# Optimization experiments

Hardware: AMD Instinct MI355X
Metric: run time of the kernel (lower is better)

## Reference

```python
import jax, jax.numpy as jnp
import numpy as np

D = 2048; H = 16; DH = D // H; FF = 8192; PFF = 1024
EPS = 1e-6; THETA = 10000.0; CAPACITY = 0.5
BETA_CE = 1.0; BETA_CU = 1.0
SCALE = 0.02

def rms(x, w):
    return x * jax.lax.rsqrt(jnp.mean(x * x, axis=-1, keepdims=True) + EPS) * w

def rope(x, pos):
    # x: [B,H,T,DH], pos: [T]
    inv = 1.0 / (THETA ** (jnp.arange(0, DH, 2, dtype=jnp.float32) / DH))
    ang = pos[:, None] * inv[None, :]                      # [T, DH/2]
    cos = jnp.concatenate([jnp.cos(ang)] * 2, -1)          # [T, DH]
    sin = jnp.concatenate([jnp.sin(ang)] * 2, -1)
    x1, x2 = jnp.split(x, 2, axis=-1)
    rot = jnp.concatenate([-x2, x1], -1)
    return x * cos + rot * sin

def attention(x, wq, wk, wv, wo):
    B, T, _ = x.shape
    pos = jnp.arange(T, dtype=jnp.float32)
    q = (x @ wq).reshape(B, T, H, DH).transpose(0, 2, 1, 3)
    k = (x @ wk).reshape(B, T, H, DH).transpose(0, 2, 1, 3)
    v = (x @ wv).reshape(B, T, H, DH).transpose(0, 2, 1, 3)
    q = rope(q, pos); k = rope(k, pos)
    scores = jnp.einsum('bhqd,bhkd->bhqk', q, k) / np.sqrt(DH).astype(np.float32)
    mask = jnp.tril(jnp.ones((T, T), dtype=bool))
    scores = jnp.where(mask, scores, jnp.finfo(scores.dtype).min)
    probs = jax.nn.softmax(scores, axis=-1)
    out = jnp.einsum('bhqk,bhkd->bhqd', probs, v)
    return out.transpose(0, 2, 1, 3).reshape(B, T, D) @ wo

def swiglu(x, wg, wu, wd):
    return (jax.nn.silu(x @ wg) * (x @ wu)) @ wd

def decoder_layer(x, ln1, ln2, wq, wk, wv, wo, wg, wu, wd):
    h = x + attention(rms(x, ln1), wq, wk, wv, wo)
    return h + swiglu(rms(h, ln2), wg, wu, wd)

def setup_inputs() -> dict:
    key = jax.random.key(0)
    ks = iter(jax.random.split(key, 32))
    def w(shape):
        return SCALE * jax.random.normal(next(ks), shape, dtype=jnp.float32)
    inp = {'hidden_states': jax.random.normal(next(ks), (2, 2048, D), dtype=jnp.float32)}
    for p in ('d1', 'd2'):
        inp[p + '_ln1'] = jnp.ones((D,), jnp.float32)
        inp[p + '_ln2'] = jnp.ones((D,), jnp.float32)
        inp[p + '_wq'] = w((D, D)); inp[p + '_wk'] = w((D, D))
        inp[p + '_wv'] = w((D, D)); inp[p + '_wo'] = w((D, D))
        inp[p + '_wg'] = w((D, FF)); inp[p + '_wu'] = w((D, FF)); inp[p + '_wd'] = w((FF, D))
    inp['p_ln'] = jnp.ones((D,), jnp.float32)
    inp['p_wg'] = w((D, PFF)); inp['p_wu'] = w((D, PFF)); inp['p_wd'] = w((PFF, D))
    return inp

def reference(hidden_states,
              d1_ln1, d1_ln2, d1_wq, d1_wk, d1_wv, d1_wo, d1_wg, d1_wu, d1_wd,
              d2_ln1, d2_ln2, d2_wq, d2_wk, d2_wv, d2_wo, d2_wg, d2_wu, d2_wd,
              p_ln, p_wg, p_wu, p_wd):
    x = hidden_states
    B, T, _ = x.shape
    # decision layer: full decoder block + prior network
    processed = decoder_layer(x, d1_ln1, d1_ln2, d1_wq, d1_wk, d1_wv, d1_wo, d1_wg, d1_wu, d1_wd)
    prior_out = swiglu(rms(x, p_ln), p_wg, p_wu, p_wd)
    prior_hidden = x + prior_out
    actual_res = processed - x                 # [B,T,D]
    pred_res = prior_out                       # prior_hidden - x
    prior_loss = jnp.mean((prior_hidden - jax.lax.stop_gradient(processed)) ** 2)
    # surprise router (VPR-style gate)
    D_st = jnp.mean(actual_res ** 2, axis=-1)                    # [B,T]
    D_ch = jnp.mean((actual_res - pred_res) ** 2, axis=-1)       # [B,T]
    g_cont = jax.nn.sigmoid(BETA_CU * D_ch - BETA_CE * D_st)     # [B,T]
    # top-k token selection per batch row
    k = max(1, int(T * CAPACITY))
    gating_scores, topk_idx = jax.lax.top_k(g_cont, k)           # [B,k]
    # gather -> process through dynamic block -> soft-gate -> scatter
    sel = jnp.take_along_axis(processed, topk_idx[..., None], axis=1)   # [B,k,D]
    sel_out = decoder_layer(sel, d2_ln1, d2_ln2, d2_wq, d2_wk, d2_wv, d2_wo, d2_wg, d2_wu, d2_wd)
    updated = sel + gating_scores[..., None] * (sel_out - sel)   # soft gating (training)
    batch_idx = jnp.arange(B)[:, None]
    final = processed.at[batch_idx, topk_idx].set(updated)
    return final, prior_loss, g_cont
```

## Files before the change

### kernel.cpp

```cpp
#include <hip/hip_runtime.h>
#include <math.h>

#define D_    2048
#define H_    16
#define DH_   128
#define FF_   8192
#define PFF_  1024
#define B_    2
#define T_    2048
#define NTOK_ 4096
#define T2_   1024
#define NSEL_ 2048
#define EPS_  1e-6f
#define SCALE_QK 0.08838834764831845f

typedef __attribute__((ext_vector_type(8))) short bf16x8;
typedef __attribute__((ext_vector_type(4))) float f32x4;
typedef __attribute__((ext_vector_type(8))) unsigned short ushort8;

__device__ __forceinline__ float silu_f(float x) {
    return x / (1.0f + expf(-x));
}

__device__ __forceinline__ unsigned short bf16_rne(float f) {
    unsigned int u = __float_as_uint(f);
    unsigned int r = (u + 0x7fffu + ((u >> 16) & 1u)) >> 16;
    return (unsigned short)r;
}
__device__ __forceinline__ float bf16_tof(unsigned short h) {
    return __uint_as_float(((unsigned int)h) << 16);
}

__global__ __launch_bounds__(256) void rms_kernel(const float* __restrict__ x,
                                                  const float* __restrict__ w,
                                                  float* __restrict__ out) {
    int row = blockIdx.x;
    int tid = threadIdx.x;
    const float4* xr = (const float4*)(x + (size_t)row * D_);
    float4* orow = (float4*)(out + (size_t)row * D_);
    const float4* w4 = (const float4*)w;
    float4 v0 = xr[tid], v1 = xr[tid + 256];
    float s = v0.x*v0.x + v0.y*v0.y + v0.z*v0.z + v0.w*v0.w
            + v1.x*v1.x + v1.y*v1.y + v1.z*v1.z + v1.w*v1.w;
    __shared__ float red[256];
    red[tid] = s; __syncthreads();
    for (int off = 128; off > 0; off >>= 1) {
        if (tid < off) red[tid] += red[tid + off];
        __syncthreads();
    }
    float r = 1.0f / sqrtf(red[0] * (1.0f/2048.0f) + EPS_);
    float4 w0 = w4[tid], w1 = w4[tid + 256];
    float4 o0, o1;
    o0.x = v0.x*r*w0.x; o0.y = v0.y*r*w0.y; o0.z = v0.z*r*w0.z; o0.w = v0.w*r*w0.w;
    o1.x = v1.x*r*w1.x; o1.y = v1.y*r*w1.y; o1.z = v1.z*r*w1.z; o1.w = v1.w*r*w1.w;
    orow[tid] = o0; orow[tid + 256] = o1;
}

__global__ __launch_bounds__(256) void splitw_kernel(const float* __restrict__ W,
                                                     unsigned short* __restrict__ phi,
                                                     unsigned short* __restrict__ plo,
                                                     int K, int N) {
    __shared__ float Ts[64][68];
    int n0 = blockIdx.x << 6, k0 = blockIdx.y << 6;
    int tid = threadIdx.x;
#pragma unroll
    for (int it = 0; it < 4; ++it) {
        int idx = tid + (it << 8);
        int kr = idx >> 4, c4 = idx & 15;
        float4 v = *(const float4*)(W + (size_t)(k0 + kr) * N + n0 + (c4 << 2));
        Ts[kr][c4*4+0] = v.x; Ts[kr][c4*4+1] = v.y; Ts[kr][c4*4+2] = v.z; Ts[kr][c4*4+3] = v.w;
    }
    __syncthreads();
#pragma unroll
    for (int h = 0; h < 2; ++h) {
        int c = tid + (h << 8);
        int kc = c >> 6, n = c & 63;
        ushort8 hi, lo;
#pragma unroll
        for (int q = 0; q < 8; ++q) {
            float v = Ts[kc*8 + q][n];
            unsigned short hb = bf16_rne(v);
            hi[q] = hb;
            lo[q] = bf16_rne(v - bf16_tof(hb));
        }
        size_t off = ((size_t)((k0 >> 3) + kc) * N + (n0 + n)) * 8;
        *(ushort8*)(phi + off) = hi;
        *(ushort8*)(plo + off) = lo;
    }
}

__global__ __launch_bounds__(256) void splita_kernel(const float* __restrict__ A,
                                                     unsigned short* __restrict__ phi,
                                                     unsigned short* __restrict__ plo,
                                                     int M, int K) {
    __shared__ float Ts[64][68];
    int m0 = blockIdx.x << 6, k0 = blockIdx.y << 6;
    int tid = threadIdx.x;
#pragma unroll
    for (int it = 0; it < 4; ++it) {
        int idx = tid + (it << 8);
        int mr = idx >> 4, c4 = idx & 15;
        float4 v = *(const float4*)(A + (size_t)(m0 + mr) * K + k0 + (c4 << 2));
        Ts[mr][c4*4+0] = v.x; Ts[mr][c4*4+1] = v.y; Ts[mr][c4*4+2] = v.z; Ts[mr][c4*4+3] = v.w;
    }
    __syncthreads();
#pragma unroll
    for (int h = 0; h < 2; ++h) {
        int c = tid + (h << 8);
        int kc = c >> 6, m = c & 63;
        const float* src = &Ts[m][kc << 3];
        ushort8 hi, lo;
#pragma unroll
        for (int q = 0; q < 8; ++q) {
            float v = src[q];
            unsigned short hb = bf16_rne(v);
            hi[q] = hb;
            lo[q] = bf16_rne(v - bf16_tof(hb));
        }
        size_t off = ((size_t)((k0 >> 3) + kc) * M + (m0 + m)) * 8;
        *(ushort8*)(phi + off) = hi;
        *(ushort8*)(plo + off) = lo;
    }
}

__device__ __forceinline__ void stage_panel(unsigned short* lds,
                                            const unsigned short* __restrict__ panel,
                                            int ktile, int R, int brow, int tid) {
#pragma unroll
    for (int h = 0; h < 2; ++h) {
        int c = tid + (h << 8);
        const unsigned short* g = panel + ((size_t)((ktile << 2) + (c >> 7)) * R + (brow + (c & 127))) * 8;
        __builtin_amdgcn_global_load_lds((const __attribute__((address_space(1))) void*)g,
                                         (__attribute__((address_space(3))) void*)(lds + (size_t)c * 8),
                                         16, 0, 0);
    }
}

template<int NP, int EPI>
__global__ __launch_bounds__(256) void gemm_mfma(const unsigned short* __restrict__ pah,
                                                 const unsigned short* __restrict__ pal,
                                                 const unsigned short* __restrict__ pbh,
                                                 const unsigned short* __restrict__ pbl,
                                                 float* __restrict__ C,
                                                 const float* __restrict__ Rg,
                                                 unsigned short* __restrict__ Cph,
                                                 unsigned short* __restrict__ Cpl,
                                                 int M, int N, int K) {
    constexpr int NPAN = (NP == 3) ? 2 : 1;
    __shared__ __align__(16) unsigned short As[2][NPAN][4][128][8];
    __shared__ __align__(16) unsigned short Bs[2][NPAN][4][128][8];
    const int tid = threadIdx.x;
    int nwg = gridDim.x * gridDim.y;
    int wg = blockIdx.y * gridDim.x + blockIdx.x;
    if ((nwg & 7) == 0) {
        int cpx = nwg >> 3;
        wg = (wg & 7) * cpx + (wg >> 3);
    }
    const int bxs = wg % gridDim.x, bys = wg / gridDim.x;
    const int bm = bys << 7, bn = bxs << 7;
    const int lane = tid & 63, wave = tid >> 6;
    const int wm = (wave >> 1) << 6, wn = (wave & 1) << 6;
    const int fr = lane & 15, fk = lane >> 4;

    f32x4 acc[4][4];
#pragma unroll
    for (int i = 0; i < 4; ++i)
#pragma unroll
        for (int j = 0; j < 4; ++j) acc[i][j] = (f32x4)0.0f;

    const int nkt = K >> 5;

    stage_panel(&As[0][0][0][0][0], pah, 0, M, bm, tid);
    if (NP == 3) stage_panel(&As[0][1][0][0][0], pal, 0, M, bm, tid);
    stage_panel(&Bs[0][0][0][0][0], pbh, 0, N, bn, tid);
    if (NP == 3) stage_panel(&Bs[0][1][0][0][0], pbl, 0, N, bn, tid);
    __syncthreads();

    int cur = 0;
    for (int kt = 0; kt < nkt; ++kt) {
        if (kt + 1 < nkt) {
            int nxt = cur ^ 1;
            stage_panel(&As[nxt][0][0][0][0], pah, kt + 1, M, bm, tid);
            if (NP == 3) stage_panel(&As[nxt][1][0][0][0], pal, kt + 1, M, bm, tid);
            stage_panel(&Bs[nxt][0][0][0][0], pbh, kt + 1, N, bn, tid);
            if (NP == 3) stage_panel(&Bs[nxt][1][0][0][0], pbl, kt + 1, N, bn, tid);
        }

        bf16x8 ah[4], bh[4], al[4], bl[4];
#pragma unroll
        for (int i = 0; i < 4; ++i) {
            ah[i] = *(const bf16x8*)&As[cur][0][fk][wm + (i << 4) + fr][0];
            if (NP == 3) al[i] = *(const bf16x8*)&As[cur][NPAN-1][fk][wm + (i << 4) + fr][0];
        }
#pragma unroll
        for (int j = 0; j < 4; ++j) {
            bh[j] = *(const bf16x8*)&Bs[cur][0][fk][wn + (j << 4) + fr][0];
            if (NP == 3) bl[j] = *(const bf16x8*)&Bs[cur][NPAN-1][fk][wn + (j << 4) + fr][0];
        }
#pragma unroll
        for (int i = 0; i < 4; ++i)
#pragma unroll
            for (int j = 0; j < 4; ++j) {
                acc[i][j] = __builtin_amdgcn_mfma_f32_16x16x32_bf16(ah[i], bh[j], acc[i][j], 0, 0, 0);
                if (NP == 3) {
                    acc[i][j] = __builtin_amdgcn_mfma_f32_16x16x32_bf16(ah[i], bl[j], acc[i][j], 0, 0, 0);
                    acc[i][j] = __builtin_amdgcn_mfma_f32_16x16x32_bf16(al[i], bh[j], acc[i][j], 0, 0, 0);
                }
            }
        __syncthreads();
        cur ^= 1;
    }

#pragma unroll
    for (int i = 0; i < 4; ++i) {
        int row0 = bm + wm + (i << 4) + (fk << 2);
#pragma unroll
        for (int j = 0; j < 4; ++j) {
            int col = bn + wn + (j << 4) + fr;
#pragma unroll
            for (int r = 0; r < 4; ++r) {
                int row = row0 + r;
                size_t off = (size_t)row * N + col;
                float v = acc[i][j][r];
                if (EPI == 0) {
                    C[off] = v;
                } else if (EPI == 1) {
                    C[off] = v + Rg[off];
                } else if (EPI == 2) {
                    C[off] = silu_f(Rg[off]) * v;
                } else {
                    v = silu_f(Rg[off]) * v;
                    unsigned short hb = bf16_rne(v);
                    size_t poff = (((size_t)(col >> 3)) * M + row) * 8 + (col & 7);
                    Cph[poff] = hb;
                    if (EPI == 3) Cpl[poff] = bf16_rne(v - bf16_tof(hb));
                }
            }
        }
    }
}

__global__ __launch_bounds__(256) void rope_split_kernel(const float* __restrict__ X,
                                                         unsigned short* __restrict__ xh,
                                                         unsigned short* __restrict__ xl,
                                                         int seqmask, float scale) {
    int tok = blockIdx.x;
    int tid = threadIdx.x;
    int h = tid >> 4, d0 = (tid & 15) << 3;
    int pos = tok & seqmask;
    const float* src = X + (size_t)tok * D_ + h * DH_;
    bool lohalf = d0 < 64;
    float out[8];
#pragma unroll
    for (int q = 0; q < 8; ++q) {
        int d = d0 + q;
        int i = lohalf ? d : (d - 64);
        float e = (float)(2 * i) * (1.0f / 128.0f);
        float inv = 1.0f / powf(10000.0f, e);
        float ang = (float)pos * inv;
        float c = cosf(ang), s = sinf(ang);
        float x1 = src[i], x2 = src[i + 64];
        out[q] = lohalf ? (x1 * c - x2 * s) : (x2 * c + x1 * s);
    }
    ushort8 hi, lo;
#pragma unroll
    for (int q = 0; q < 8; ++q) {
        float v = out[q] * scale;
        unsigned short hb = bf16_rne(v);
        hi[q] = hb;
        lo[q] = bf16_rne(v - bf16_tof(hb));
    }
    size_t off = (size_t)tok * D_ + h * DH_ + d0;
    *(ushort8*)(xh + off) = hi;
    *(ushort8*)(xl + off) = lo;
}

__global__ __launch_bounds__(256) void vpack_kernel(const float* __restrict__ V,
                                                    unsigned short* __restrict__ vth,
                                                    unsigned short* __restrict__ vtl,
                                                    int T) {
    __shared__ float Ts[64][132];
    int kt = blockIdx.x, bh = blockIdx.y;
    int b = bh >> 4, h = bh & 15;
    int tid = threadIdx.x;
#pragma unroll
    for (int it = 0; it < 8; ++it) {
        int idx = tid + (it << 8);
        int r = idx >> 5, c4 = idx & 31;
        float4 v = *(const float4*)(V + ((size_t)(b * T + kt * 64 + r)) * D_ + h * DH_ + (c4 << 2));
        Ts[r][c4*4+0] = v.x; Ts[r][c4*4+1] = v.y; Ts[r][c4*4+2] = v.z; Ts[r][c4*4+3] = v.w;
    }
    __syncthreads();
    size_t obase = ((size_t)bh * (size_t)(T >> 3) + (size_t)kt * 8) * 1024;
#pragma unroll
    for (int it = 0; it < 4; ++it) {
        int c = tid + (it << 8);
        int kc = c >> 7, dh = c & 127;
        ushort8 hi, lo;
#pragma unroll
        for (int q = 0; q < 8; ++q) {
            float v = Ts[kc * 8 + q][dh];
            unsigned short hb = bf16_rne(v);
            hi[q] = hb;
            lo[q] = bf16_rne(v - bf16_tof(hb));
        }
        *(ushort8*)(vth + obase + (size_t)kc * 1024 + dh * 8) = hi;
        *(ushort8*)(vtl + obase + (size_t)kc * 1024 + dh * 8) = lo;
    }
}

__global__ __launch_bounds__(256) void attn_mfma(const unsigned short* __restrict__ QH,
                                                 const unsigned short* __restrict__ QL,
                                                 const unsigned short* __restrict__ KH,
                                                 const unsigned short* __restrict__ KL,
                                                 const unsigned short* __restrict__ VTH,
                                                 const unsigned short* __restrict__ VTL,
                                                 float* __restrict__ O, int T) {
    __shared__ __align__(16) unsigned short KV[16384];
    __shared__ __align__(16) float Ss[4096];
    __shared__ __align__(16) float mrow[64];
    __shared__ __align__(16) float lrow[64];
    __shared__ __align__(16) float crow[64];

    const int tid = threadIdx.x;
    const int qt = blockIdx.x, bh = blockIdx.y;
    const int b = bh >> 4, h = bh & 15;
    const int lane = tid & 63, w = tid >> 6;
    const int fr = lane & 15, fk = lane >> 4;
    const size_t tok0 = (size_t)b * T;

    char* lds_kv = (char*)&KV[0];
    char* lds_sp = (char*)&Ss[0];

    bf16x8 qfh[4], qfl[4];
    {
        const size_t qoff = (tok0 + (size_t)qt * 64 + w * 16 + fr) * D_ + h * DH_ + fk * 8;
#pragma unroll
        for (int ks = 0; ks < 4; ++ks) {
            qfh[ks] = *(const bf16x8*)(QH + qoff + ks * 32);
            qfl[ks] = *(const bf16x8*)(QL + qoff + ks * 32);
        }
    }
    if (tid < 64) { mrow[tid] = -1e30f; lrow[tid] = 0.f; }

    f32x4 acc[8];
#pragma unroll
    for (int nt = 0; nt < 8; ++nt) acc[nt] = (f32x4)0.f;

    const int srow = tid >> 2, sslot = tid & 3;
    const size_t vbase = (size_t)bh * (size_t)(T >> 3) * 1024;

    for (int kt = 0; kt <= qt; ++kt) {
        __syncthreads();
#pragma unroll
        for (int it = 0; it < 4; ++it) {
            int c = tid + (it << 8);
            int t = c >> 4;
            int sp = (c & 15) ^ (t & 7);
            size_t goff = (tok0 + (size_t)kt * 64 + t) * D_ + h * DH_ + sp * 8;
            __builtin_amdgcn_global_load_lds((const __attribute__((address_space(1))) void*)(KH + goff),
                (__attribute__((address_space(3))) void*)(lds_kv + c * 16), 16, 0, 0);
            __builtin_amdgcn_global_load_lds((const __attribute__((address_space(1))) void*)(KL + goff),
                (__attribute__((address_space(3))) void*)(lds_kv + 16384 + c * 16), 16, 0, 0);
        }
        __syncthreads();
        {
            f32x4 s[4];
#pragma unroll
            for (int nt = 0; nt < 4; ++nt) s[nt] = (f32x4)0.f;
#pragma unroll
            for (int ks = 0; ks < 4; ++ks) {
#pragma unroll
                for (int nt = 0; nt < 4; ++nt) {
                    int n = nt * 16 + fr;
                    int offk = (n * 256 + ks * 64 + fk * 16) ^ ((n & 7) << 4);
                    bf16x8 kfh = *(const bf16x8*)(lds_kv + offk);
                    bf16x8 kfl = *(const bf16x8*)(lds_kv + 16384 + offk);
                    s[nt] = __builtin_amdgcn_mfma_f32_16x16x32_bf16(qfh[ks], kfh, s[nt], 0, 0, 0);
                    s[nt] = __builtin_amdgcn_mfma_f32_16x16x32_bf16(qfh[ks], kfl, s[nt], 0, 0, 0);
                    s[nt] = __builtin_amdgcn_mfma_f32_16x16x32_bf16(qfl[ks], kfh, s[nt], 0, 0, 0);
                }
            }
#pragma unroll
            for (int nt = 0; nt < 4; ++nt)
#pragma unroll
                for (int r = 0; r < 4; ++r) {
                    int row = w * 16 + fk * 4 + r;
                    int col = nt * 16 + fr;
                    *(float*)(lds_sp + ((row * 256 + col * 4) ^ ((row & 7) << 4))) = s[nt][r];
                }
        }
        __syncthreads();
#pragma unroll
        for (int it = 0; it < 4; ++it) {
            int c = tid + (it << 8);
            size_t goff = vbase + (size_t)kt * 8192 + (size_t)c * 8;
            __builtin_amdgcn_global_load_lds((const __attribute__((address_space(1))) void*)(VTH + goff),
                (__attribute__((address_space(3))) void*)(lds_kv + c * 16), 16, 0, 0);
            __builtin_amdgcn_global_load_lds((const __attribute__((address_space(1))) void*)(VTL + goff),
                (__attribute__((address_space(3))) void*)(lds_kv + 16384 + c * 16), 16, 0, 0);
        }
        float p[16];
        float newm, psum, cr, oldl;
        {
            float tmax = -1e30f;
            int colbase = sslot * 16;
#pragma unroll
            for (int q4 = 0; q4 < 4; ++q4) {
                f32x4 sv = *(const f32x4*)(lds_sp + ((srow * 256 + sslot * 64 + q4 * 16) ^ ((srow & 7) << 4)));
#pragma unroll
                for (int e = 0; e < 4; ++e) {
                    float v = sv[e];
                    if (kt == qt && (colbase + q4 * 4 + e) > srow) v = -1e30f;
                    p[q4 * 4 + e] = v;
                    tmax = fmaxf(tmax, v);
                }
            }
            tmax = fmaxf(tmax, __shfl_xor(tmax, 1, 64));
            tmax = fmaxf(tmax, __shfl_xor(tmax, 2, 64));
            float oldm = mrow[srow];
            oldl = lrow[srow];
            newm = fmaxf(oldm, tmax);
            psum = 0.f;
#pragma unroll
            for (int e = 0; e < 16; ++e) { p[e] = expf(p[e] - newm); psum += p[e]; }
            psum += __shfl_xor(psum, 1, 64);
            psum += __shfl_xor(psum, 2, 64);
            cr = expf(oldm - newm);
        }
        __syncthreads();
        {
            ushort8 h0, h1, l0, l1;
#pragma unroll
            for (int e = 0; e < 8; ++e) {
                unsigned short hb = bf16_rne(p[e]);
                h0[e] = hb; l0[e] = bf16_rne(p[e] - bf16_tof(hb));
                unsigned short hb2 = bf16_rne(p[8 + e]);
                h1[e] = hb2; l1[e] = bf16_rne(p[8 + e] - bf16_tof(hb2));
            }
            int base = srow * 128 + sslot * 32;
            int swz = (srow & 7) << 4;
            *(ushort8*)(lds_sp + (base ^ swz)) = h0;
            *(ushort8*)(lds_sp + ((base + 16) ^ swz)) = h1;
            *(ushort8*)(lds_sp + 8192 + (base ^ swz)) = l0;
            *(ushort8*)(lds_sp + 8192 + ((base + 16) ^ swz)) = l1;
            if (sslot == 0) { mrow[srow] = newm; lrow[srow] = oldl * cr + psum; crow[srow] = cr; }
        }
        __syncthreads();
        {
            f32x4 crv = *(const f32x4*)&crow[w * 16 + fk * 4];
#pragma unroll
            for (int nt = 0; nt < 8; ++nt)
#pragma unroll
                for (int r = 0; r < 4; ++r) acc[nt][r] *= crv[r];
            int m = w * 16 + fr;
#pragma unroll
            for (int ks = 0; ks < 2; ++ks) {
                int offp = (m * 128 + ks * 64 + fk * 16) ^ ((m & 7) << 4);
                bf16x8 pfh = *(const bf16x8*)(lds_sp + offp);
                bf16x8 pfl = *(const bf16x8*)(lds_sp + 8192 + offp);
#pragma unroll
                for (int nt = 0; nt < 8; ++nt) {
                    int offv = (ks * 4 + fk) * 2048 + (nt * 16 + fr) * 16;
                    bf16x8 vfh = *(const bf16x8*)(lds_kv + offv);
                    bf16x8 vfl = *(const bf16x8*)(lds_kv + 16384 + offv);
                    acc[nt] = __builtin_amdgcn_mfma_f32_16x16x32_bf16(pfh, vfh, acc[nt], 0, 0, 0);
                    acc[nt] = __builtin_amdgcn_mfma_f32_16x16x32_bf16(pfh, vfl, acc[nt], 0, 0, 0);
                    acc[nt] = __builtin_amdgcn_mfma_f32_16x16x32_bf16(pfl, vfh, acc[nt], 0, 0, 0);
                }
            }
        }
    }
    __syncthreads();
    {
        f32x4 lv = *(const f32x4*)&lrow[w * 16 + fk * 4];
        float* orow = O + (tok0 + (size_t)qt * 64 + w * 16 + fk * 4) * D_ + h * DH_;
#pragma unroll
        for (int r = 0; r < 4; ++r) {
            float inv = 1.0f / lv[r];
#pragma unroll
            for (int nt = 0; nt < 8; ++nt)
                orow[(size_t)r * D_ + nt * 16 + fr] = acc[nt][r] * inv;
        }
    }
}

template<int EPI>
__global__ __launch_bounds__(256) void gemm128(const float* __restrict__ A,
                                               const float* __restrict__ Bm,
                                               float* __restrict__ C,
                                               const float* __restrict__ Rg,
                                               int M, int N, int K) {
    __shared__ float Ast[16][132];
    __shared__ float Bs[16][132];
    int bm = blockIdx.y << 7, bn = blockIdx.x << 7;
    int tid = threadIdx.x;
    int ty = tid >> 4, tx = tid & 15;
    float acc[8][8];
#pragma unroll
    for (int i = 0; i < 8; ++i)
#pragma unroll
        for (int j = 0; j < 8; ++j) acc[i][j] = 0.f;

    for (int k0 = 0; k0 < K; k0 += 16) {
#pragma unroll
        for (int it = 0; it < 2; ++it) {
            int idx = tid + (it << 8);
            int ar = idx >> 2, ac = idx & 3;
            float4 av = *(const float4*)(A + (size_t)(bm + ar) * K + k0 + (ac << 2));
            Ast[ac*4+0][ar] = av.x; Ast[ac*4+1][ar] = av.y;
            Ast[ac*4+2][ar] = av.z; Ast[ac*4+3][ar] = av.w;
            int br = idx >> 5, bc = idx & 31;
            float4 bv = *(const float4*)(Bm + (size_t)(k0 + br) * N + bn + (bc << 2));
            *(float4*)&Bs[br][bc << 2] = bv;
        }
        __syncthreads();
#pragma unroll
        for (int kk = 0; kk < 16; ++kk) {
            float a[8], b[8];
            *(float4*)&a[0] = *(const float4*)&Ast[kk][ty*4];
            *(float4*)&a[4] = *(const float4*)&Ast[kk][64 + ty*4];
            *(float4*)&b[0] = *(const float4*)&Bs[kk][tx*4];
            *(float4*)&b[4] = *(const float4*)&Bs[kk][64 + tx*4];
#pragma unroll
            for (int i = 0; i < 8; ++i)
#pragma unroll
                for (int j = 0; j < 8; ++j)
                    acc[i][j] += a[i] * b[j];
        }
        __syncthreads();
    }
#pragma unroll
    for (int i = 0; i < 8; ++i) {
        int row = bm + ((i < 4) ? (ty*4 + i) : (64 + ty*4 + (i - 4)));
#pragma unroll
        for (int half = 0; half < 2; ++half) {
            int col = bn + half*64 + tx*4;
            size_t off = (size_t)row * N + col;
            const float* ap = &acc[i][half*4];
            float4 r;
            if (EPI == 0) {
                r.x = ap[0]; r.y = ap[1]; r.z = ap[2]; r.w = ap[3];
            } else if (EPI == 1) {
                float4 rv = *(const float4*)(Rg + off);
                r.x = ap[0] + rv.x; r.y = ap[1] + rv.y;
                r.z = ap[2] + rv.z; r.w = ap[3] + rv.w;
            } else {
                float4 gv = *(const float4*)(Rg + off);
                r.x = silu_f(gv.x) * ap[0]; r.y = silu_f(gv.y) * ap[1];
                r.z = silu_f(gv.z) * ap[2]; r.w = silu_f(gv.w) * ap[3];
            }
            *(float4*)(C + off) = r;
        }
    }
}

__global__ __launch_bounds__(256) void rope_kernel(float* __restrict__ q, int nrows, int seqlen) {
    int gid = blockIdx.x * 256 + threadIdx.x;
    int tok = gid >> 10;
    if (tok >= nrows) return;
    int rest = gid & 1023;
    int h = rest >> 6, i = rest & 63;
    int pos = tok % seqlen;
    float e = (float)(2 * i) * (1.0f / 128.0f);
    float inv = 1.0f / powf(10000.0f, e);
    float ang = (float)pos * inv;
    float c = cosf(ang), s = sinf(ang);
    size_t base = (size_t)tok * D_ + h * 128 + i;
    float x1 = q[base], x2 = q[base + 64];
    q[base]      = x1 * c - x2 * s;
    q[base + 64] = x2 * c + x1 * s;
}

__global__ __launch_bounds__(256) void attn_kernel(const float* __restrict__ Q,
                                                   const float* __restrict__ K,
                                                   const float* __restrict__ V,
                                                   float* __restrict__ O,
                                                   int T) {
    int qt = blockIdx.x;
    int bh = blockIdx.y;
    int b = bh >> 4, h = bh & 15;
    int tid = threadIdx.x;

    __shared__ float4 Qs[32][32];
    __shared__ float4 KVs[64][32];
    __shared__ float Sst[32][65];
    __shared__ float mrow[32], lrow[32], crow[32];

    const size_t headoff = (size_t)h * DH_;
    const size_t bbase = (size_t)b * T * D_;

#pragma unroll
    for (int i = 0; i < 4; ++i) {
        int idx = tid + i * 256;
        int r = idx >> 5, ch = idx & 31;
        const float4* src = (const float4*)(Q + bbase + (size_t)(qt*32 + r) * D_ + headoff);
        Qs[r][ch ^ ((r >> 2) & 7)] = src[ch];
    }
    if (tid < 32) { mrow[tid] = -1e30f; lrow[tid] = 0.f; }

    int ty16 = tid >> 4, tx16 = tid & 15;
    int r8 = tid >> 3, q8 = tid & 7;
    float o[2][8];
#pragma unroll
    for (int i = 0; i < 2; ++i)
#pragma unroll
        for (int j = 0; j < 8; ++j) o[i][j] = 0.f;

    int ktmax = (qt * 32 + 31) >> 6;
    for (int kt = 0; kt <= ktmax; ++kt) {
        __syncthreads();
#pragma unroll
        for (int i = 0; i < 8; ++i) {
            int idx = tid + i * 256;
            int r = idx >> 5, ch = idx & 31;
            const float4* src = (const float4*)(K + bbase + (size_t)(kt*64 + r) * D_ + headoff);
            KVs[r][ch ^ ((r >> 2) & 7)] = src[ch];
        }
        __syncthreads();
        {
            float s[2][4];
#pragma unroll
            for (int i = 0; i < 2; ++i)
#pragma unroll
                for (int j = 0; j < 4; ++j) s[i][j] = 0.f;
#pragma unroll
            for (int ch = 0; ch < 32; ++ch) {
                float4 qv[2], kv[4];
#pragma unroll
                for (int i = 0; i < 2; ++i) { int r = ty16*2 + i; qv[i] = Qs[r][ch ^ ((r >> 2) & 7)]; }
#pragma unroll
                for (int j = 0; j < 4; ++j) { int c = tx16*4 + j; kv[j] = KVs[c][ch ^ ((c >> 2) & 7)]; }
#pragma unroll
                for (int i = 0; i < 2; ++i)
#pragma unroll
                    for (int j = 0; j < 4; ++j)
                        s[i][j] += qv[i].x*kv[j].x + qv[i].y*kv[j].y + qv[i].z*kv[j].z + qv[i].w*kv[j].w;
            }
#pragma unroll
            for (int i = 0; i < 2; ++i) {
                int grow = qt*32 + ty16*2 + i;
#pragma unroll
                for (int j = 0; j < 4; ++j) {
                    int gcol = kt*64 + tx16*4 + j;
                    float sv = s[i][j] * SCALE_QK;
                    if (gcol > grow) sv = -1e30f;
                    Sst[ty16*2 + i][tx16*4 + j] = sv;
                }
            }
        }
        __syncthreads();
#pragma unroll
        for (int i = 0; i < 8; ++i) {
            int idx = tid + i * 256;
            int r = idx >> 5, ch = idx & 31;
            const float4* src = (const float4*)(V + bbase + (size_t)(kt*64 + r) * D_ + headoff);
            KVs[r][ch ^ ((r >> 2) & 7)] = src[ch];
        }
        {
            float pv[8];
            float tmax = -1e30f;
#pragma unroll
            for (int c = 0; c < 8; ++c) { pv[c] = Sst[r8][q8*8 + c]; tmax = fmaxf(tmax, pv[c]); }
#pragma unroll
            for (int m = 1; m < 8; m <<= 1) tmax = fmaxf(tmax, __shfl_xor(tmax, m, 64));
            float oldm = mrow[r8];
            float newm = fmaxf(oldm, tmax);
            float psum = 0.f;
#pragma unroll
            for (int c = 0; c < 8; ++c) {
                float p = expf(pv[c] - newm);
                Sst[r8][q8*8 + c] = p;
                psum += p;
            }
#pragma unroll
            for (int m = 1; m < 8; m <<= 1) psum += __shfl_xor(psum, m, 64);
            if (q8 == 0) {
                float crv = expf(oldm - newm);
                crow[r8] = crv;
                lrow[r8] = lrow[r8] * crv + psum;
                mrow[r8] = newm;
            }
        }
        __syncthreads();
        {
            float crv[2];
#pragma unroll
            for (int i = 0; i < 2; ++i) {
                crv[i] = crow[ty16*2 + i];
#pragma unroll
                for (int j = 0; j < 8; ++j) o[i][j] *= crv[i];
            }
#pragma unroll
            for (int kc = 0; kc < 64; ++kc) {
                int swz = (kc >> 2) & 7;
                float4 v0 = KVs[kc][tx16 ^ swz];
                float4 v1 = KVs[kc][(16 + tx16) ^ swz];
#pragma unroll
                for (int i = 0; i < 2; ++i) {
                    float p = Sst[ty16*2 + i][kc];
                    o[i][0] += p*v0.x; o[i][1] += p*v0.y; o[i][2] += p*v0.z; o[i][3] += p*v0.w;
                    o[i][4] += p*v1.x; o[i][5] += p*v1.y; o[i][6] += p*v1.z; o[i][7] += p*v1.w;
                }
            }
        }
    }
#pragma unroll
    for (int i = 0; i < 2; ++i) {
        int r = ty16*2 + i;
        float inv = 1.0f / lrow[r];
        float4 a, bb;
        a.x = o[i][0]*inv; a.y = o[i][1]*inv; a.z = o[i][2]*inv; a.w = o[i][3]*inv;
        bb.x = o[i][4]*inv; bb.y = o[i][5]*inv; bb.z = o[i][6]*inv; bb.w = o[i][7]*inv;
        float* dst = O + bbase + (size_t)(qt*32 + r) * D_ + headoff;
        ((float4*)dst)[tx16] = a;
        ((float4*)dst)[16 + tx16] = bb;
    }
}

__global__ __launch_bounds__(256) void router_kernel(const float* __restrict__ x,
                                                     const float* __restrict__ proc,
                                                     const float* __restrict__ prior,
                                                     float* __restrict__ gbuf,
                                                     float* __restrict__ dchbuf,
                                                     float* __restrict__ gout) {
    int row = blockIdx.x, tid = threadIdx.x;
    const float4* x4 = (const float4*)(x + (size_t)row * D_);
    const float4* p4 = (const float4*)(proc + (size_t)row * D_);
    const float4* r4 = (const float4*)(prior + (size_t)row * D_);
    float sst = 0.f, sch = 0.f;
#pragma unroll
    for (int it = 0; it < 2; ++it) {
        int i = tid + it * 256;
        float4 xv = x4[i], pv = p4[i], rv = r4[i];
        float a0 = pv.x - xv.x, a1 = pv.y - xv.y, a2 = pv.z - xv.z, a3 = pv.w - xv.w;
        sst += a0*a0 + a1*a1 + a2*a2 + a3*a3;
        float d0 = a0 - rv.x, d1 = a1 - rv.y, d2 = a2 - rv.z, d3 = a3 - rv.w;
        sch += d0*d0 + d1*d1 + d2*d2 + d3*d3;
    }
    __shared__ float rs[256], rc[256];
    rs[tid] = sst; rc[tid] = sch; __syncthreads();
    for (int off = 128; off > 0; off >>= 1) {
        if (tid < off) { rs[tid] += rs[tid + off]; rc[tid] += rc[tid + off]; }
        __syncthreads();
    }
    if (tid == 0) {
        float Dst = rs[0] * (1.0f/2048.0f);
        float Dch = rc[0] * (1.0f/2048.0f);
        float g = 1.0f / (1.0f + expf(-(Dch - Dst)));
        gbuf[row] = g; dchbuf[row] = Dch; gout[row] = g;
    }
}

__global__ __launch_bounds__(1024) void loss_kernel(const float* __restrict__ dch, float* __restrict__ out) {
    __shared__ float red[1024];
    int tid = threadIdx.x;
    red[tid] = dch[tid] + dch[tid + 1024] + dch[tid + 2048] + dch[tid + 3072];
    __syncthreads();
    for (int off = 512; off > 0; off >>= 1) {
        if (tid < off) red[tid] += red[tid + off];
        __syncthreads();
    }
    if (tid == 0) out[0] = red[0] * (1.0f / 4096.0f);
}

__global__ __launch_bounds__(1024) void topk_kernel(const float* __restrict__ gbuf,
                                                    int* __restrict__ idxout,
                                                    float* __restrict__ gateout) {
    int b = blockIdx.x, tid = threadIdx.x;
    __shared__ float val[2048];
    __shared__ int idx[2048];
    val[tid] = gbuf[b*2048 + tid];           idx[tid] = tid;
    val[tid + 1024] = gbuf[b*2048 + tid + 1024]; idx[tid + 1024] = tid + 1024;
    __syncthreads();
    for (int kk = 2; kk <= 2048; kk <<= 1) {
        for (int j = kk >> 1; j > 0; j >>= 1) {
            for (int i = tid; i < 2048; i += 1024) {
                int ixj = i ^ j;
                if (ixj > i) {
                    bool up = ((i & kk) == 0);
                    float v1 = val[i], v2 = val[ixj];
                    int i1 = idx[i], i2 = idx[ixj];
                    bool sw = up ? ((v2 > v1) || (v2 == v1 && i2 < i1))
                                 : ((v1 > v2) || (v1 == v2 && i1 < i2));
                    if (sw) { val[i] = v2; val[ixj] = v1; idx[i] = i2; idx[ixj] = i1; }
                }
            }
            __syncthreads();
        }
    }
    if (tid < 1024) {
        idxout[b*1024 + tid] = idx[tid];
        gateout[b*1024 + tid] = val[tid];
    }
}

__global__ __launch_bounds__(256) void gather_kernel(const float* __restrict__ proc,
                                                     const int* __restrict__ idx,
                                                     float* __restrict__ sel) {
    int r = blockIdx.x;
    int b = r >> 10, rr = r & 1023;
    int tok = idx[b*1024 + rr];
    const float4* src = (const float4*)(proc + ((size_t)(b*2048 + tok)) * D_);
    float4* dst = (float4*)(sel + (size_t)r * D_);
    dst[threadIdx.x] = src[threadIdx.x];
    dst[threadIdx.x + 256] = src[threadIdx.x + 256];
}

__global__ __launch_bounds__(256) void copy_kernel(const float* __restrict__ src,
                                                   float* __restrict__ dst, int n4) {
    int i = blockIdx.x * 256 + threadIdx.x;
    if (i < n4) ((float4*)dst)[i] = ((const float4*)src)[i];
}

__global__ __launch_bounds__(256) void scatter_kernel(const float* __restrict__ sel,
                                                      const float* __restrict__ selout,
                                                      const int* __restrict__ idx,
                                                      const float* __restrict__ gate,
                                                      float* __restrict__ outp) {
    int r = blockIdx.x;
    int b = r >> 10, rr = r & 1023;
    int tok = idx[b*1024 + rr];
    float g = gate[b*1024 + rr];
    const float4* s4 = (const float4*)(sel + (size_t)r * D_);
    const float4* o4 = (const float4*)(selout + (size_t)r * D_);
    float4* d4 = (float4*)(outp + ((size_t)(b*2048 + tok)) * D_);
#pragma unroll
    for (int it = 0; it < 2; ++it) {
        int i = threadIdx.x + it * 256;
        float4 a = s4[i], o = o4[i];
        float4 w;
        w.x = a.x + g*(o.x - a.x); w.y = a.y + g*(o.y - a.y);
        w.z = a.z + g*(o.z - a.z); w.w = a.w + g*(o.w - a.w);
        d4[i] = w;
    }
}

extern "C" void kernel_launch(void* const* d_in, const int* in_sizes, int n_in,
                              void* d_out, int out_size, void* d_ws, size_t ws_size,
                              hipStream_t stream) {
    const float* X      = (const float*)d_in[0];
    const float* d1_ln1 = (const float*)d_in[1];
    const float* d1_ln2 = (const float*)d_in[2];
    const float* d1_wq  = (const float*)d_in[3];
    const float* d1_wk  = (const float*)d_in[4];
    const float* d1_wv  = (const float*)d_in[5];
    const float* d1_wo  = (const float*)d_in[6];
    const float* d1_wg  = (const float*)d_in[7];
    const float* d1_wu  = (const float*)d_in[8];
    const float* d1_wd  = (const float*)d_in[9];
    const float* d2_ln1 = (const float*)d_in[10];
    const float* d2_ln2 = (const float*)d_in[11];
    const float* d2_wq  = (const float*)d_in[12];
    const float* d2_wk  = (const float*)d_in[13];
    const float* d2_wv  = (const float*)d_in[14];
    const float* d2_wo  = (const float*)d_in[15];
    const float* d2_wg  = (const float*)d_in[16];
    const float* d2_wu  = (const float*)d_in[17];
    const float* d2_wd  = (const float*)d_in[18];
    const float* p_ln   = (const float*)d_in[19];
    const float* p_wg   = (const float*)d_in[20];
    const float* p_wu   = (const float*)d_in[21];
    const float* p_wd   = (const float*)d_in[22];

    float* out = (float*)d_out;
    float* ws  = (float*)d_ws;

    const size_t BIG = (size_t)NTOK_ * D_;
    const size_t MEG = 1024 * 1024;

    const size_t NEED_NEW = (128 * MEG + 16384) * 4;
    const size_t NEED_OLD = ((5*BIG + (size_t)NTOK_*FF_ + 12288) * 4);

    if (ws_size >= NEED_NEW) {
        float* BUF0 = ws;
        float* BUF1 = ws + 8*MEG;
        float* BUF2 = ws + 16*MEG;
        float* BUF3 = ws + 24*MEG;
        float* BUF4 = ws + 32*MEG;
        float* BUFF = ws + 40*MEG;
        unsigned short* PWhi  = (unsigned short*)(ws + 72*MEG);
        unsigned short* PWlo  = (unsigned short*)(ws + 80*MEG);
        unsigned short* PAhi  = (unsigned short*)(ws + 88*MEG);
        unsigned short* PAlo  = (unsigned short*)(ws + 92*MEG);
        unsigned short* PFhi  = (unsigned short*)(ws + 96*MEG);
        unsigned short* PFlo  = (unsigned short*)(ws + 112*MEG);
        unsigned short* U   = (unsigned short*)(ws + 96*MEG);
        const size_t PK = (size_t)NTOK_ * D_;
        unsigned short* QHp = U;
        unsigned short* QLp = U + PK;
        unsigned short* KHp = U + 2*PK;
        unsigned short* KLp = U + 3*PK;
        unsigned short* VTH = U + 4*PK;
        unsigned short* VTL = U + 5*PK;
        float* SM   = ws + 128*MEG;
        float* gbuf = SM;
        float* dch  = SM + 4096;
        float* gate = SM + 8192;
        int*   idxb = (int*)(SM + 10240);

        rms_kernel<<<NTOK_, 256, 0, stream>>>(X, d1_ln1, BUF0);
        splita_kernel<<<dim3(64, 32), 256, 0, stream>>>(BUF0, PAhi, PAlo, NTOK_, D_);
        splitw_kernel<<<dim3(32, 32), 256, 0, stream>>>(d1_wq, PWhi, PWlo, D_, D_);
        gemm_mfma<3,0><<<dim3(16, 32), 256, 0, stream>>>(PAhi, PAlo, PWhi, PWlo, BUF1, nullptr, nullptr, nullptr, NTOK_, D_, D_);
        splitw_kernel<<<dim3(32, 32), 256, 0, stream>>>(d1_wk, PWhi, PWlo, D_, D_);
        gemm_mfma<3,0><<<dim3(16, 32), 256, 0, stream>>>(PAhi, PAlo, PWhi, PWlo, BUF2, nullptr, nullptr, nullptr, NTOK_, D_, D_);
        splitw_kernel<<<dim3(32, 32), 256, 0, stream>>>(d1_wv, PWhi, PWlo, D_, D_);
        gemm_mfma<3,0><<<dim3(16, 32), 256, 0, stream>>>(PAhi, PAlo, PWhi, PWlo, BUF3, nullptr, nullptr, nullptr, NTOK_, D_, D_);
        rope_split_kernel<<<NTOK_, 256, 0, stream>>>(BUF1, QHp, QLp, T_ - 1, SCALE_QK);
        rope_split_kernel<<<NTOK_, 256, 0, stream>>>(BUF2, KHp, KLp, T_ - 1, 1.0f);
        vpack_kernel<<<dim3(T_/64, B_*H_), 256, 0, stream>>>(BUF3, VTH, VTL, T_);
        attn_mfma<<<dim3(T_/64, B_*H_), 256, 0, stream>>>(QHp, QLp, KHp, KLp, VTH, VTL, BUF4, T_);
        splita_kernel<<<dim3(64, 32), 256, 0, stream>>>(BUF4, PAhi, PAlo, NTOK_, D_);
        splitw_kernel<<<dim3(32, 32), 256, 0, stream>>>(d1_wo, PWhi, PWlo, D_, D_);
        gemm_mfma<3,1><<<dim3(16, 32), 256, 0, stream>>>(PAhi, PAlo, PWhi, PWlo, BUF2, X, nullptr, nullptr, NTOK_, D_, D_);
        rms_kernel<<<NTOK_, 256, 0, stream>>>(BUF2, d1_ln2, BUF0);
        splita_kernel<<<dim3(64, 32), 256, 0, stream>>>(BUF0, PAhi, PAlo, NTOK_, D_);
        splitw_kernel<<<dim3(128, 32), 256, 0, stream>>>(d1_wg, PWhi, PWlo, D_, FF_);
        gemm_mfma<3,0><<<dim3(64, 32), 256, 0, stream>>>(PAhi, PAlo, PWhi, PWlo, BUFF, nullptr, nullptr, nullptr, NTOK_, FF_, D_);
        splitw_kernel<<<dim3(128, 32), 256, 0, stream>>>(d1_wu, PWhi, PWlo, D_, FF_);
        gemm_mfma<3,3><<<dim3(64, 32), 256, 0, stream>>>(PAhi, PAlo, PWhi, PWlo, nullptr, BUFF, PFhi, PFlo, NTOK_, FF_, D_);
        splitw_kernel<<<dim3(32, 128), 256, 0, stream>>>(d1_wd, PWhi, PWlo, FF_, D_);
        gemm_mfma<3,1><<<dim3(16, 32), 256, 0, stream>>>(PFhi, PFlo, PWhi, PWlo, BUF1, BUF2, nullptr, nullptr, NTOK_, D_, FF_);

        rms_kernel<<<NTOK_, 256, 0, stream>>>(X, p_ln, BUF0);
        splita_kernel<<<dim3(64, 32), 256, 0, stream>>>(BUF0, PAhi, PAlo, NTOK_, D_);
        splitw_kernel<<<dim3(16, 32), 256, 0, stream>>>(p_wg, PWhi, PWlo, D_, PFF_);
        gemm_mfma<3,0><<<dim3(8, 32), 256, 0, stream>>>(PAhi, PAlo, PWhi, PWlo, BUFF, nullptr, nullptr, nullptr, NTOK_, PFF_, D_);
        splitw_kernel<<<dim3(16, 32), 256, 0, stream>>>(p_wu, PWhi, PWlo, D_, PFF_);
        gemm_mfma<3,3><<<dim3(8, 32), 256, 0, stream>>>(PAhi, PAlo, PWhi, PWlo, nullptr, BUFF, PFhi, PFlo, NTOK_, PFF_, D_);
        splitw_kernel<<<dim3(32, 16), 256, 0, stream>>>(p_wd, PWhi, PWlo, PFF_, D_);
        gemm_mfma<3,0><<<dim3(16, 32), 256, 0, stream>>>(PFhi, PFlo, PWhi, PWlo, BUF3, nullptr, nullptr, nullptr, NTOK_, D_, PFF_);

        router_kernel<<<NTOK_, 256, 0, stream>>>(X, BUF1, BUF3, gbuf, dch, out + 8388609);
        loss_kernel<<<1, 1024, 0, stream>>>(dch, out + 8388608);
        topk_kernel<<<B_, 1024, 0, stream>>>(gbuf, idxb, gate);
        gather_kernel<<<NSEL_, 256, 0, stream>>>(BUF1, idxb, BUF4);

        float* V2 = BUF4 + (size_t)NSEL_ * D_;
        rms_kernel<<<NSEL_, 256, 0, stream>>>(BUF4, d2_ln1, BUF0);
        splita_kernel<<<dim3(32, 32), 256, 0, stream>>>(BUF0, PAhi, PAlo, NSEL_, D_);
        splitw_kernel<<<dim3(32, 32), 256, 0, stream>>>(d2_wq, PWhi, PWlo, D_, D_);
        gemm_mfma<1,0><<<dim3(16, 16), 256, 0, stream>>>(PAhi, PAlo, PWhi, PWlo, BUF2, nullptr, nullptr, nullptr, NSEL_, D_, D_);
        splitw_kernel<<<dim3(32, 32), 256, 0, stream>>>(d2_wk, PWhi, PWlo, D_, D_);
        gemm_mfma<1,0><<<dim3(16, 16), 256, 0, stream>>>(PAhi, PAlo, PWhi, PWlo, BUF3, nullptr, nullptr, nullptr, NSEL_, D_, D_);
        splitw_kernel<<<dim3(32, 32), 256, 0, stream>>>(d2_wv, PWhi, PWlo, D_, D_);
        gemm_mfma<1,0><<<dim3(16, 16), 256, 0, stream>>>(PAhi, PAlo, PWhi, PWlo, V2, nullptr, nullptr, nullptr, NSEL_, D_, D_);
        rope_split_kernel<<<NSEL_, 256, 0, stream>>>(BUF2, QHp, QLp, T2_ - 1, SCALE_QK);
        rope_split_kernel<<<NSEL_, 256, 0, stream>>>(BUF3, KHp, KLp, T2_ - 1, 1.0f);
        vpack_kernel<<<dim3(T2_/64, B_*H_), 256, 0, stream>>>(V2, VTH, VTL, T2_);
        attn_mfma<<<dim3(T2_/64, B_*H_), 256, 0, stream>>>(QHp, QLp, KHp, KLp, VTH, VTL, BUF0, T2_);
        splita_kernel<<<dim3(32, 32), 256, 0, stream>>>(BUF0, PAhi, PAlo, NSEL_, D_);
        splitw_kernel<<<dim3(32, 32), 256, 0, stream>>>(d2_wo, PWhi, PWlo, D_, D_);
        gemm_mfma<1,1><<<dim3(16, 16), 256, 0, stream>>>(PAhi, PAlo, PWhi, PWlo, BUF2, BUF4, nullptr, nullptr, NSEL_, D_, D_);
        rms_kernel<<<NSEL_, 256, 0, stream>>>(BUF2, d2_ln2, BUF0);
        splita_kernel<<<dim3(32, 32), 256, 0, stream>>>(BUF0, PAhi, PAlo, NSEL_, D_);
        splitw_kernel<<<dim3(128, 32), 256, 0, stream>>>(d2_wg, PWhi, PWlo, D_, FF_);
        gemm_mfma<1,0><<<dim3(64, 16), 256, 0, stream>>>(PAhi, PAlo, PWhi, PWlo, BUFF, nullptr, nullptr, nullptr, NSEL_, FF_, D_);
        splitw_kernel<<<dim3(128, 32), 256, 0, stream>>>(d2_wu, PWhi, PWlo, D_, FF_);
        gemm_mfma<1,4><<<dim3(64, 16), 256, 0, stream>>>(PAhi, PAlo, PWhi, PWlo, nullptr, BUFF, PFhi, nullptr, NSEL_, FF_, D_);
        splitw_kernel<<<dim3(32, 128), 256, 0, stream>>>(d2_wd, PWhi, PWlo, FF_, D_);
        gemm_mfma<1,1><<<dim3(16, 16), 256, 0, stream>>>(PFhi, PFlo, PWhi, PWlo, BUF3, BUF2, nullptr, nullptr, NSEL_, D_, FF_);

        copy_kernel<<<8192, 256, 0, stream>>>(BUF1, out, (int)(BIG / 4));
        scatter_kernel<<<NSEL_, 256, 0, stream>>>(BUF4, BUF3, idxb, gate, out);
        return;
    }

    if (ws_size < NEED_OLD) return;

    float* BUF0 = ws;
    float* BUF1 = ws + BIG;
    float* BUF2 = ws + 2*BIG;
    float* BUF3 = ws + 3*BIG;
    float* BUF4 = ws + 4*BIG;
    float* BUFF = ws + 5*BIG;
    float* SM   = BUFF + (size_t)NTOK_ * FF_;
    float* gbuf = SM;
    float* dch  = SM + 4096;
    float* gate = SM + 8192;
    int*   idxb = (int*)(SM + 10240);

    rms_kernel<<<NTOK_, 256, 0, stream>>>(X, d1_ln1, BUF0);
    gemm128<0><<<dim3(16, 32), 256, 0, stream>>>(BUF0, d1_wq, BUF1, nullptr, NTOK_, D_, D_);
    gemm128<0><<<dim3(16, 32), 256, 0, stream>>>(BUF0, d1_wk, BUF2, nullptr, NTOK_, D_, D_);
    gemm128<0><<<dim3(16, 32), 256, 0, stream>>>(BUF0, d1_wv, BUF3, nullptr, NTOK_, D_, D_);
    rope_kernel<<<NTOK_*4, 256, 0, stream>>>(BUF1, NTOK_, T_);
    rope_kernel<<<NTOK_*4, 256, 0, stream>>>(BUF2, NTOK_, T_);
    attn_kernel<<<dim3(T_/32, B_*H_), 256, 0, stream>>>(BUF1, BUF2, BUF3, BUF4, T_);
    gemm128<1><<<dim3(16, 32), 256, 0, stream>>>(BUF4, d1_wo, BUF2, X, NTOK_, D_, D_);
    rms_kernel<<<NTOK_, 256, 0, stream>>>(BUF2, d1_ln2, BUF0);
    gemm128<0><<<dim3(64, 32), 256, 0, stream>>>(BUF0, d1_wg, BUFF, nullptr, NTOK_, FF_, D_);
    gemm128<2><<<dim3(64, 32), 256, 0, stream>>>(BUF0, d1_wu, BUFF, BUFF, NTOK_, FF_, D_);
    gemm128<1><<<dim3(16, 32), 256, 0, stream>>>(BUFF, d1_wd, BUF1, BUF2, NTOK_, D_, FF_);

    rms_kernel<<<NTOK_, 256, 0, stream>>>(X, p_ln, BUF0);
    gemm128<0><<<dim3(8, 32), 256, 0, stream>>>(BUF0, p_wg, BUF4, nullptr, NTOK_, PFF_, D_);
    gemm128<2><<<dim3(8, 32), 256, 0, stream>>>(BUF0, p_wu, BUF4, BUF4, NTOK_, PFF_, D_);
    gemm128<0><<<dim3(16, 32), 256, 0, stream>>>(BUF4, p_wd, BUF3, nullptr, NTOK_, D_, PFF_);

    router_kernel<<<NTOK_, 256, 0, stream>>>(X, BUF1, BUF3, gbuf, dch, out + 8388609);
    loss_kernel<<<1, 1024, 0, stream>>>(dch, out + 8388608);
    topk_kernel<<<B_, 1024, 0, stream>>>(gbuf, idxb, gate);
    gather_kernel<<<NSEL_, 256, 0, stream>>>(BUF1, idxb, BUF4);

    float* V2 = BUF4 + (size_t)NSEL_ * D_;
    rms_kernel<<<NSEL_, 256, 0, stream>>>(BUF4, d2_ln1, BUF0);
    gemm128<0><<<dim3(16, 16), 256, 0, stream>>>(BUF0, d2_wq, BUF2, nullptr, NSEL_, D_, D_);
    gemm128<0><<<dim3(16, 16), 256, 0, stream>>>(BUF0, d2_wk, BUF3, nullptr, NSEL_, D_, D_);
    gemm128<0><<<dim3(16, 16), 256, 0, stream>>>(BUF0, d2_wv, V2, nullptr, NSEL_, D_, D_);
    rope_kernel<<<NSEL_*4, 256, 0, stream>>>(BUF2, NSEL_, T2_);
    rope_kernel<<<NSEL_*4, 256, 0, stream>>>(BUF3, NSEL_, T2_);
    attn_kernel<<<dim3(T2_/32, B_*H_), 256, 0, stream>>>(BUF2, BUF3, V2, BUF0, T2_);
    gemm128<1><<<dim3(16, 16), 256, 0, stream>>>(BUF0, d2_wo, BUF2, BUF4, NSEL_, D_, D_);
    rms_kernel<<<NSEL_, 256, 0, stream>>>(BUF2, d2_ln2, BUF0);
    gemm128<0><<<dim3(64, 16), 256, 0, stream>>>(BUF0, d2_wg, BUFF, nullptr, NSEL_, FF_, D_);
    gemm128<2><<<dim3(64, 16), 256, 0, stream>>>(BUF0, d2_wu, BUFF, BUFF, NSEL_, FF_, D_);
    gemm128<1><<<dim3(16, 16), 256, 0, stream>>>(BUFF, d2_wd, BUF3, BUF2, NSEL_, D_, FF_);

    copy_kernel<<<8192, 256, 0, stream>>>(BUF1, out, (int)(BIG / 4));
    scatter_kernel<<<NSEL_, 256, 0, stream>>>(BUF4, BUF3, idxb, gate, out);
}
```

Measured before the change: 3.214 ms.

## Write processed output directly into out and single-buffer GEMM LDS staging

The first decoder layer's down-projection GEMM now writes its result straight into the output buffer. The router and gather read from there, which removes the final full-tensor copy kernel. Separately, the GEMM's LDS double buffering is removed: each k-tile is loaded, synchronized and then computed, halving shared memory per block. That may raise occupancy, but global-to-LDS loads no longer overlap with MFMA work, and each iteration now has an extra barrier.

New measurement: 3.389 ms. +5.4%, slower.

```diff
diff --git a/kernel.cpp b/kernel.cpp
--- a/kernel.cpp
+++ b/kernel.cpp
@@ -147,8 +147,8 @@
                                                  unsigned short* __restrict__ Cpl,
                                                  int M, int N, int K) {
     constexpr int NPAN = (NP == 3) ? 2 : 1;
-    __shared__ __align__(16) unsigned short As[2][NPAN][4][128][8];
-    __shared__ __align__(16) unsigned short Bs[2][NPAN][4][128][8];
+    __shared__ __align__(16) unsigned short As[NPAN][4][128][8];
+    __shared__ __align__(16) unsigned short Bs[NPAN][4][128][8];
     const int tid = threadIdx.x;
     int nwg = gridDim.x * gridDim.y;
     int wg = blockIdx.y * gridDim.x + blockIdx.x;
@@ -169,33 +169,23 @@
         for (int j = 0; j < 4; ++j) acc[i][j] = (f32x4)0.0f;
 
     const int nkt = K >> 5;
-
-    stage_panel(&As[0][0][0][0][0], pah, 0, M, bm, tid);
-    if (NP == 3) stage_panel(&As[0][1][0][0][0], pal, 0, M, bm, tid);
-    stage_panel(&Bs[0][0][0][0][0], pbh, 0, N, bn, tid);
-    if (NP == 3) stage_panel(&Bs[0][1][0][0][0], pbl, 0, N, bn, tid);
-    __syncthreads();
-
-    int cur = 0;
     for (int kt = 0; kt < nkt; ++kt) {
-        if (kt + 1 < nkt) {
-            int nxt = cur ^ 1;
-            stage_panel(&As[nxt][0][0][0][0], pah, kt + 1, M, bm, tid);
-            if (NP == 3) stage_panel(&As[nxt][1][0][0][0], pal, kt + 1, M, bm, tid);
-            stage_panel(&Bs[nxt][0][0][0][0], pbh, kt + 1, N, bn, tid);
-            if (NP == 3) stage_panel(&Bs[nxt][1][0][0][0], pbl, kt + 1, N, bn, tid);
-        }
+        stage_panel(&As[0][0][0][0], pah, kt, M, bm, tid);
+        if (NP == 3) stage_panel(&As[NPAN-1][0][0][0], pal, kt, M, bm, tid);
+        stage_panel(&Bs[0][0][0][0], pbh, kt, N, bn, tid);
+        if (NP == 3) stage_panel(&Bs[NPAN-1][0][0][0], pbl, kt, N, bn, tid);
+        __syncthreads();
 
         bf16x8 ah[4], bh[4], al[4], bl[4];
 #pragma unroll
         for (int i = 0; i < 4; ++i) {
-            ah[i] = *(const bf16x8*)&As[cur][0][fk][wm + (i << 4) + fr][0];
-            if (NP == 3) al[i] = *(const bf16x8*)&As[cur][NPAN-1][fk][wm + (i << 4) + fr][0];
+            ah[i] = *(const bf16x8*)&As[0][fk][wm + (i << 4) + fr][0];
+            if (NP == 3) al[i] = *(const bf16x8*)&As[NPAN-1][fk][wm + (i << 4) + fr][0];
         }
 #pragma unroll
         for (int j = 0; j < 4; ++j) {
-            bh[j] = *(const bf16x8*)&Bs[cur][0][fk][wn + (j << 4) + fr][0];
-            if (NP == 3) bl[j] = *(const bf16x8*)&Bs[cur][NPAN-1][fk][wn + (j << 4) + fr][0];
+            bh[j] = *(const bf16x8*)&Bs[0][fk][wn + (j << 4) + fr][0];
+            if (NP == 3) bl[j] = *(const bf16x8*)&Bs[NPAN-1][fk][wn + (j << 4) + fr][0];
         }
 #pragma unroll
         for (int i = 0; i < 4; ++i)
@@ -208,7 +198,6 @@
                 }
             }
         __syncthreads();
-        cur ^= 1;
     }
 
 #pragma unroll
@@ -899,6 +888,8 @@
         float* gate = SM + 8192;
         int*   idxb = (int*)(SM + 10240);
 
+        float* PROC = out;
+
         rms_kernel<<<NTOK_, 256, 0, stream>>>(X, d1_ln1, BUF0);
         splita_kernel<<<dim3(64, 32), 256, 0, stream>>>(BUF0, PAhi, PAlo, NTOK_, D_);
         splitw_kernel<<<dim3(32, 32), 256, 0, stream>>>(d1_wq, PWhi, PWlo, D_, D_);
@@ -921,7 +912,7 @@
         splitw_kernel<<<dim3(128, 32), 256, 0, stream>>>(d1_wu, PWhi, PWlo, D_, FF_);
         gemm_mfma<3,3><<<dim3(64, 32), 256, 0, stream>>>(PAhi, PAlo, PWhi, PWlo, nullptr, BUFF, PFhi, PFlo, NTOK_, FF_, D_);
         splitw_kernel<<<dim3(32, 128), 256, 0, stream>>>(d1_wd, PWhi, PWlo, FF_, D_);
-        gemm_mfma<3,1><<<dim3(16, 32), 256, 0, stream>>>(PFhi, PFlo, PWhi, PWlo, BUF1, BUF2, nullptr, nullptr, NTOK_, D_, FF_);
+        gemm_mfma<3,1><<<dim3(16, 32), 256, 0, stream>>>(PFhi, PFlo, PWhi, PWlo, PROC, BUF2, nullptr, nullptr, NTOK_, D_, FF_);
 
         rms_kernel<<<NTOK_, 256, 0, stream>>>(X, p_ln, BUF0);
         splita_kernel<<<dim3(64, 32), 256, 0, stream>>>(BUF0, PAhi, PAlo, NTOK_, D_);
@@ -932,10 +923,10 @@
         splitw_kernel<<<dim3(32, 16), 256, 0, stream>>>(p_wd, PWhi, PWlo, PFF_, D_);
         gemm_mfma<3,0><<<dim3(16, 32), 256, 0, stream>>>(PFhi, PFlo, PWhi, PWlo, BUF3, nullptr, nullptr, nullptr, NTOK_, D_, PFF_);
 
-        router_kernel<<<NTOK_, 256, 0, stream>>>(X, BUF1, BUF3, gbuf, dch, out + 8388609);
+        router_kernel<<<NTOK_, 256, 0, stream>>>(X, PROC, BUF3, gbuf, dch, out + 8388609);
         loss_kernel<<<1, 1024, 0, stream>>>(dch, out + 8388608);
         topk_kernel<<<B_, 1024, 0, stream>>>(gbuf, idxb, gate);
-        gather_kernel<<<NSEL_, 256, 0, stream>>>(BUF1, idxb, BUF4);
+        gather_kernel<<<NSEL_, 256, 0, stream>>>(PROC, idxb, BUF4);
 
         float* V2 = BUF4 + (size_t)NSEL_ * D_;
         rms_kernel<<<NSEL_, 256, 0, stream>>>(BUF4, d2_ln1, BUF0);
@@ -962,7 +953,6 @@
         splitw_kernel<<<dim3(32, 128), 256, 0, stream>>>(d2_wd, PWhi, PWlo, FF_, D_);
         gemm_mfma<1,1><<<dim3(16, 16), 256, 0, stream>>>(PFhi, PFlo, PWhi, PWlo, BUF3, BUF2, nullptr, nullptr, NSEL_, D_, FF_);
 
-        copy_kernel<<<8192, 256, 0, stream>>>(BUF1, out, (int)(BIG / 4));
         scatter_kernel<<<NSEL_, 256, 0, stream>>>(BUF4, BUF3, idxb, gate, out);
         return;
     }
```
